# Performance work log

Measured on AMD Instinct MI355X. Metric: run time of the kernel, lower is better.

The kernel has to match this reference:

```python
import jax, jax.numpy as jnp
import numpy as np
import math

L = 3        # n_layers
H = 8        # n_heads
D = 128      # embed_dim
KD = D // H  # key_dim = val_dim = 16
FF = 512     # feed_forward_hidden
B, N = 200, 100
BN = B * N
E = 320000
EPS = 1e-5   # BatchNorm1d eps


def setup_inputs() -> dict:
    key = jax.random.key(0)
    ks = jax.random.split(key, 12)

    def u(k, shape, last):  # torch uniform(-1/sqrt(last), 1/sqrt(last)) init
        s = 1.0 / math.sqrt(last)
        return jax.random.uniform(k, shape, jnp.float32, -s, s)

    x = jax.random.normal(ks[0], (B, N, D), jnp.float32)
    edge_index = jax.random.randint(ks[1], (2, E), 0, BN, jnp.int32)
    return {
        "x": x,
        "edge_index": edge_index,
        "Wq": u(ks[2], (L, H, D, KD), KD),
        "Wk": u(ks[3], (L, H, D, KD), KD),
        "Wv": u(ks[4], (L, H, D, KD), KD),
        "Wout": u(ks[5], (L, H, KD, D), D),
        "bn1_w": jnp.ones((L, D), jnp.float32),
        "bn1_b": jnp.zeros((L, D), jnp.float32),
        "W1": u(ks[6], (L, D, FF), D),
        "b1": u(ks[7], (L, FF), D),
        "W2": u(ks[8], (L, FF, D), FF),
        "b2": u(ks[9], (L, D), FF),
        "bn2_w": jnp.ones((L, D), jnp.float32),
        "bn2_b": jnp.zeros((L, D), jnp.float32),
    }


def _batch_norm(h, w, b):
    # BatchNorm1d over flattened (B*N, D), training-mode batch stats (biased var)
    flat = h.reshape(-1, h.shape[-1])
    mu = flat.mean(axis=0)
    var = flat.var(axis=0)
    y = (flat - mu) / jnp.sqrt(var + EPS) * w + b
    return y.reshape(h.shape)


def _gat_conv(h, src, dst, Wq, Wk, Wv, Wout):
    Bb, Nn, Dd = h.shape
    bn = Bb * Nn
    flat = h.reshape(bn, Dd)
    Hh, _, Kk = Wq.shape
    # faithful to torch: matmul gives [H, BN, K], then raw .view(BN, H, K)
    Q = jnp.einsum('nd,hdk->hnk', flat, Wq).reshape(bn, Hh, Kk)
    Kt = jnp.einsum('nd,hdk->hnk', flat, Wk).reshape(bn, Hh, Kk)
    V = jnp.einsum('nd,hdk->hnk', flat, Wv).reshape(bn, Hh, Kk)
    norm = 1.0 / math.sqrt(Kk)
    # message: Q_j (source) . K_i (target) per edge, per head -> [E, H]
    attn = norm * jnp.sum(Q[src] * Kt[dst], axis=-1)
    # segment softmax over edges grouped by target node (max detached, as in PyG)
    m = jax.lax.stop_gradient(jax.ops.segment_max(attn, dst, num_segments=bn))
    ex = jnp.exp(attn - m[dst])
    s = jax.ops.segment_sum(ex, dst, num_segments=bn)
    a = ex / (s[dst] + 1e-16)
    # weighted V_i scatter-added into target nodes -> [BN, H, K]
    aggr = jax.ops.segment_sum(V[dst] * a[:, :, None], dst, num_segments=bn)
    out = aggr.reshape(bn, Hh * Kk) @ Wout.reshape(Hh * Kk, -1)
    return out.reshape(Bb, Nn, -1)


def reference(x, edge_index, Wq, Wk, Wv, Wout, bn1_w, bn1_b, W1, b1, W2, b2, bn2_w, bn2_b):
    src, dst = edge_index[0], edge_index[1]
    h = x
    for l in range(L):
        h = h + _gat_conv(h, src, dst, Wq[l], Wk[l], Wv[l], Wout[l])
        h = _batch_norm(h, bn1_w[l], bn1_b[l])
        ff = jnp.maximum(h @ W1[l] + b1[l], 0.0) @ W2[l] + b2[l]
        h = h + ff
        h = _batch_norm(h, bn2_w[l], bn2_b[l])
    return h
```

## Files before the change

### kernel.cpp

```cpp
#include <hip/hip_runtime.h>
#include <hip/hip_bf16.h>

#define BN_ 20000
#define D_ 128
#define FF_ 512
#define E_ 320000
#define NBLK 313
#define LSTR 136
#define TSTR 72
#define B2STR 72

typedef __attribute__((ext_vector_type(8))) short bf16x8;
typedef __attribute__((ext_vector_type(4))) float f32x4;

__device__ __forceinline__ unsigned short f2b(float f) {
    unsigned int u = __float_as_uint(f);
    u = (u + 0x7FFFu + ((u >> 16) & 1u)) >> 16;
    return (unsigned short)u;
}

__device__ __forceinline__ void make_ss(const float* __restrict__ acc,
                                        const float* __restrict__ w,
                                        const float* __restrict__ b,
                                        float* __restrict__ ss_sh, int tid) {
    if (tid < 128) {
        if (acc) {
            float s = acc[tid], q = acc[128 + tid];
            float mu  = s * (1.f / 20000.f);
            float var = fmaxf(q * (1.f / 20000.f) - mu * mu, 0.f);
            float rstd  = rsqrtf(var + 1e-5f);
            float scale = w[tid] * rstd;
            ss_sh[tid]       = scale;
            ss_sh[128 + tid] = b[tid] - mu * scale;
        } else {
            ss_sh[tid]       = 1.f;
            ss_sh[128 + tid] = 0.f;
        }
    }
}

__global__ __launch_bounds__(256) void k_prep(const float* __restrict__ Wv,
                                              const float* __restrict__ Wout,
                                              const float* __restrict__ W1,
                                              const float* __restrict__ W2,
                                              const int* __restrict__ dst,
                                              unsigned short* __restrict__ WcT,
                                              unsigned short* __restrict__ WoT,
                                              unsigned short* __restrict__ W1T,
                                              unsigned short* __restrict__ W2T,
                                              float* __restrict__ flag,
                                              float* __restrict__ acc6) {
    const int gid = blockIdx.x * 256 + threadIdx.x;
    const int gs = 1250 * 256;
    for (int idx = gid; idx < 49152; idx += gs) {
        int l = idx / 16384, r = idx % 16384;
        int n = r >> 7, k = r & 127;
        int h = n >> 4, kk = n & 15;
        WcT[idx] = f2b(Wv[((l * 8 + h) * 128 + k) * 16 + kk]);
    }
    for (int idx = gid; idx < 49152; idx += gs) {
        int l = idx / 16384, r = idx % 16384;
        int n = r >> 7, k = r & 127;
        WoT[idx] = f2b(Wout[l * 16384 + k * 128 + n]);
    }
    for (int idx = gid; idx < 196608; idx += gs) {
        int l = idx / 65536, r = idx % 65536;
        int n = r >> 7, k = r & 127;
        W1T[idx] = f2b(W1[l * 65536 + k * 512 + n]);
    }
    for (int idx = gid; idx < 196608; idx += gs) {
        int l = idx / 65536, r = idx % 65536;
        int n = r / 512, k = r % 512;
        W2T[idx] = f2b(W2[l * 65536 + k * 128 + n]);
    }
    if (gid < 1536) acc6[gid] = 0.f;
    if (gid < E_) flag[dst[gid]] = 1.0f;
}


__global__ __launch_bounds__(256) void k_vs(const float* __restrict__ H,
                                            const float* __restrict__ accP,
                                            const float* __restrict__ bnw,
                                            const float* __restrict__ bnb,
                                            const unsigned short* __restrict__ Bt,
                                            unsigned short* __restrict__ Vs) {
    __shared__ unsigned short As[64 * LSTR];
    __shared__ unsigned short Bs[64 * LSTR];
    __shared__ float ss_sh[256];
    const int tid = threadIdx.x;
    const int row0 = blockIdx.x * 64, col0 = blockIdx.y * 64;
    make_ss(accP, bnw, bnb, ss_sh, tid);
    __syncthreads();
#pragma unroll
    for (int it = 0; it < 4; ++it) {
        int idx = tid + it * 256;
        int m = idx >> 4, k0 = (idx & 15) << 3;
        int gr = row0 + m;
        float v[8];
        if (gr < BN_) {
            f32x4 v0 = *(const f32x4*)(H + gr * D_ + k0);
            f32x4 v1 = *(const f32x4*)(H + gr * D_ + k0 + 4);
            v[0] = v0.x; v[1] = v0.y; v[2] = v0.z; v[3] = v0.w;
            v[4] = v1.x; v[5] = v1.y; v[6] = v1.z; v[7] = v1.w;
        } else {
#pragma unroll
            for (int j = 0; j < 8; ++j) v[j] = 0.f;
        }
        unsigned int p[4];
#pragma unroll
        for (int j = 0; j < 4; ++j) {
            unsigned short lo = f2b(v[2 * j] * ss_sh[k0 + 2 * j] + ss_sh[128 + k0 + 2 * j]);
            unsigned short hi = f2b(v[2 * j + 1] * ss_sh[k0 + 2 * j + 1] + ss_sh[128 + k0 + 2 * j + 1]);
            p[j] = (unsigned int)lo | ((unsigned int)hi << 16);
        }
        *(uint4*)&As[m * LSTR + k0] = make_uint4(p[0], p[1], p[2], p[3]);
    }
#pragma unroll
    for (int it = 0; it < 4; ++it) {
        int idx = tid + it * 256;
        int n = idx >> 4, k0 = (idx & 15) << 3;
        *(uint4*)&Bs[n * LSTR + k0] = *(const uint4*)(Bt + (col0 + n) * D_ + k0);
    }
    __syncthreads();
    const int lane = tid & 63, wave = tid >> 6;
    const int l16 = lane & 15, quad = lane >> 4;
    const int wm = (wave >> 1) * 32, wn = (wave & 1) * 32;
    f32x4 acc[2][2] = {};
#pragma unroll
    for (int kb = 0; kb < 128; kb += 32) {
        bf16x8 a0 = *(bf16x8*)&As[(wm + l16) * LSTR + kb + quad * 8];
        bf16x8 a1 = *(bf16x8*)&As[(wm + 16 + l16) * LSTR + kb + quad * 8];
        bf16x8 b0 = *(bf16x8*)&Bs[(wn + l16) * LSTR + kb + quad * 8];
        bf16x8 b1 = *(bf16x8*)&Bs[(wn + 16 + l16) * LSTR + kb + quad * 8];
        acc[0][0] = __builtin_amdgcn_mfma_f32_16x16x32_bf16(a0, b0, acc[0][0], 0, 0, 0);
        acc[0][1] = __builtin_amdgcn_mfma_f32_16x16x32_bf16(a0, b1, acc[0][1], 0, 0, 0);
        acc[1][0] = __builtin_amdgcn_mfma_f32_16x16x32_bf16(a1, b0, acc[1][0], 0, 0, 0);
        acc[1][1] = __builtin_amdgcn_mfma_f32_16x16x32_bf16(a1, b1, acc[1][1], 0, 0, 0);
    }
#pragma unroll
    for (int i = 0; i < 2; ++i)
#pragma unroll
        for (int j = 0; j < 2; ++j) {
            int gc = col0 + wn + j * 16 + l16;
            int h = gc >> 4, kk = gc & 15;
#pragma unroll
            for (int r = 0; r < 4; ++r) {
                int gr = row0 + wm + i * 16 + quad * 4 + r;
                if (gr < BN_) Vs[h * (BN_ * 16) + gr * 16 + kk] = f2b(acc[i][j][r]);
            }
        }
}

__global__ __launch_bounds__(256) void k_out(const unsigned short* __restrict__ Vs,
                                             const unsigned short* __restrict__ Bt,
                                             const float* __restrict__ H,
                                             const float* __restrict__ accP,
                                             const float* __restrict__ bnw,
                                             const float* __restrict__ bnb,
                                             const float* __restrict__ flag,
                                             float* __restrict__ H1,
                                             float* __restrict__ accO) {
    __shared__ unsigned short As[64 * LSTR];
    __shared__ unsigned short Bs[64 * LSTR];
    __shared__ float ss_sh[256];
    const int tid = threadIdx.x;
    const int row0 = blockIdx.x * 64, col0 = blockIdx.y * 64;
    make_ss(accP, bnw, bnb, ss_sh, tid);
#pragma unroll
    for (int it = 0; it < 4; ++it) {
        int idx = tid + it * 256;
        int m = idx >> 4, k0 = (idx & 15) << 3;
        int gr = row0 + m;
        uint4 w = make_uint4(0u, 0u, 0u, 0u);
        if (gr < BN_) w = *(const uint4*)(Vs + gr * D_ + k0);
        *(uint4*)&As[m * LSTR + k0] = w;
    }
#pragma unroll
    for (int it = 0; it < 4; ++it) {
        int idx = tid + it * 256;
        int n = idx >> 4, k0 = (idx & 15) << 3;
        *(uint4*)&Bs[n * LSTR + k0] = *(const uint4*)(Bt + (col0 + n) * D_ + k0);
    }
    __syncthreads();
    const int lane = tid & 63, wave = tid >> 6;
    const int l16 = lane & 15, quad = lane >> 4;
    const int wm = (wave >> 1) * 32, wn = (wave & 1) * 32;
    f32x4 acc[2][2] = {};
#pragma unroll
    for (int kb = 0; kb < 128; kb += 32) {
        bf16x8 a0 = *(bf16x8*)&As[(wm + l16) * LSTR + kb + quad * 8];
        bf16x8 a1 = *(bf16x8*)&As[(wm + 16 + l16) * LSTR + kb + quad * 8];
        bf16x8 b0 = *(bf16x8*)&Bs[(wn + l16) * LSTR + kb + quad * 8];
        bf16x8 b1 = *(bf16x8*)&Bs[(wn + 16 + l16) * LSTR + kb + quad * 8];
        acc[0][0] = __builtin_amdgcn_mfma_f32_16x16x32_bf16(a0, b0, acc[0][0], 0, 0, 0);
        acc[0][1] = __builtin_amdgcn_mfma_f32_16x16x32_bf16(a0, b1, acc[0][1], 0, 0, 0);
        acc[1][0] = __builtin_amdgcn_mfma_f32_16x16x32_bf16(a1, b0, acc[1][0], 0, 0, 0);
        acc[1][1] = __builtin_amdgcn_mfma_f32_16x16x32_bf16(a1, b1, acc[1][1], 0, 0, 0);
    }
    __syncthreads();
    float* Sred = (float*)As;
    float* Qred = (float*)Bs;
    const int slot = (wave >> 1) * 4 + quad;
#pragma unroll
    for (int j = 0; j < 2; ++j) {
        int gc = col0 + wn + j * 16 + l16;
        float sc = ss_sh[gc & 127];
        float sh = ss_sh[128 + (gc & 127)];
        float cs = 0.f, cq = 0.f;
#pragma unroll
        for (int i = 0; i < 2; ++i)
#pragma unroll
            for (int r = 0; r < 4; ++r) {
                int gr = row0 + wm + i * 16 + quad * 4 + r;
                if (gr < BN_) {
                    float z = H[gr * D_ + gc] * sc + sh;
                    float o = z + flag[gr] * acc[i][j][r];
                    H1[gr * D_ + gc] = o;
                    cs += o; cq += o * o;
                }
            }
        Sred[(wn + j * 16 + l16) * 8 + slot] = cs;
        Qred[(wn + j * 16 + l16) * 8 + slot] = cq;
    }
    __syncthreads();
    if (tid < 64) {
        float s = 0.f, q = 0.f;
#pragma unroll
        for (int t = 0; t < 8; ++t) { s += Sred[tid * 8 + t]; q += Qred[tid * 8 + t]; }
        atomicAdd(&accO[col0 + tid], s);
        atomicAdd(&accO[128 + col0 + tid], q);
    }
}

__global__ __launch_bounds__(256) void k_ff(const float* __restrict__ H1,
                                            const float* __restrict__ accP,
                                            const float* __restrict__ bnw,
                                            const float* __restrict__ bnb,
                                            const unsigned short* __restrict__ W1t,
                                            const float* __restrict__ b1l,
                                            const unsigned short* __restrict__ W2t,
                                            const float* __restrict__ b2l,
                                            float* __restrict__ H2,
                                            float* __restrict__ accO) {
    __shared__ unsigned short As[64 * LSTR];
    __shared__ unsigned short Bs[64 * LSTR];
    __shared__ unsigned short B2[128 * B2STR];
    __shared__ unsigned short Tch[64 * TSTR];
    __shared__ float ss_sh[256];
    const int tid = threadIdx.x;
    const int row0 = blockIdx.x * 64;
    make_ss(accP, bnw, bnb, ss_sh, tid);
    __syncthreads();
#pragma unroll
    for (int it = 0; it < 4; ++it) {
        int idx = tid + it * 256;
        int m = idx >> 4, k0 = (idx & 15) << 3;
        int gr = row0 + m;
        float v[8];
        if (gr < BN_) {
            f32x4 v0 = *(const f32x4*)(H1 + gr * D_ + k0);
            f32x4 v1 = *(const f32x4*)(H1 + gr * D_ + k0 + 4);
            v[0] = v0.x; v[1] = v0.y; v[2] = v0.z; v[3] = v0.w;
            v[4] = v1.x; v[5] = v1.y; v[6] = v1.z; v[7] = v1.w;
        } else {
#pragma unroll
            for (int j = 0; j < 8; ++j) v[j] = 0.f;
        }
        unsigned int p[4];
#pragma unroll
        for (int j = 0; j < 4; ++j) {
            unsigned short lo = f2b(v[2 * j] * ss_sh[k0 + 2 * j] + ss_sh[128 + k0 + 2 * j]);
            unsigned short hi = f2b(v[2 * j + 1] * ss_sh[k0 + 2 * j + 1] + ss_sh[128 + k0 + 2 * j + 1]);
            p[j] = (unsigned int)lo | ((unsigned int)hi << 16);
        }
        *(uint4*)&As[m * LSTR + k0] = make_uint4(p[0], p[1], p[2], p[3]);
    }
    const int lane = tid & 63, wave = tid >> 6;
    const int l16 = lane & 15, quad = lane >> 4;
    const int wm = (wave >> 1) * 32;
    const int wn = (wave & 1) * 32;
    const int wn2 = (wave & 1) * 64;
    f32x4 acc2[2][4] = {};
    for (int c = 0; c < 8; ++c) {
        const int cb = c * 64;
        __syncthreads();
#pragma unroll
        for (int it = 0; it < 4; ++it) {
            int idx = tid + it * 256;
            int n = idx >> 4, k0 = (idx & 15) << 3;
            *(uint4*)&Bs[n * LSTR + k0] = *(const uint4*)(W1t + (cb + n) * D_ + k0);
        }
#pragma unroll
        for (int it = 0; it < 4; ++it) {
            int idx = tid + it * 256;
            int n = idx >> 3, k0 = (idx & 7) << 3;
            *(uint4*)&B2[n * B2STR + k0] = *(const uint4*)(W2t + n * FF_ + cb + k0);
        }
        __syncthreads();
        f32x4 acc1[2][2] = {};
#pragma unroll
        for (int kb = 0; kb < 128; kb += 32) {
            bf16x8 a0 = *(bf16x8*)&As[(wm + l16) * LSTR + kb + quad * 8];
            bf16x8 a1 = *(bf16x8*)&As[(wm + 16 + l16) * LSTR + kb + quad * 8];
            bf16x8 b0 = *(bf16x8*)&Bs[(wn + l16) * LSTR + kb + quad * 8];
            bf16x8 b1 = *(bf16x8*)&Bs[(wn + 16 + l16) * LSTR + kb + quad * 8];
            acc1[0][0] = __builtin_amdgcn_mfma_f32_16x16x32_bf16(a0, b0, acc1[0][0], 0, 0, 0);
            acc1[0][1] = __builtin_amdgcn_mfma_f32_16x16x32_bf16(a0, b1, acc1[0][1], 0, 0, 0);
            acc1[1][0] = __builtin_amdgcn_mfma_f32_16x16x32_bf16(a1, b0, acc1[1][0], 0, 0, 0);
            acc1[1][1] = __builtin_amdgcn_mfma_f32_16x16x32_bf16(a1, b1, acc1[1][1], 0, 0, 0);
        }
#pragma unroll
        for (int j = 0; j < 2; ++j) {
            int lc = wn + j * 16 + l16;
            float bb = b1l[cb + lc];
#pragma unroll
            for (int i = 0; i < 2; ++i)
#pragma unroll
                for (int r = 0; r < 4; ++r)
                    Tch[(wm + i * 16 + quad * 4 + r) * TSTR + lc] =
                        f2b(fmaxf(acc1[i][j][r] + bb, 0.f));
        }
        __syncthreads();
#pragma unroll
        for (int kb = 0; kb < 64; kb += 32) {
            bf16x8 a0 = *(bf16x8*)&Tch[(wm + l16) * TSTR + kb + quad * 8];
            bf16x8 a1 = *(bf16x8*)&Tch[(wm + 16 + l16) * TSTR + kb + quad * 8];
#pragma unroll
            for (int j2 = 0; j2 < 4; ++j2) {
                bf16x8 b = *(bf16x8*)&B2[(wn2 + j2 * 16 + l16) * B2STR + kb + quad * 8];
                acc2[0][j2] = __builtin_amdgcn_mfma_f32_16x16x32_bf16(a0, b, acc2[0][j2], 0, 0, 0);
                acc2[1][j2] = __builtin_amdgcn_mfma_f32_16x16x32_bf16(a1, b, acc2[1][j2], 0, 0, 0);
            }
        }
    }
    __syncthreads();
    float* Sred = (float*)As;
    float* Qred = (float*)Bs;
    const int slot = (wave >> 1) * 4 + quad;
#pragma unroll
    for (int j2 = 0; j2 < 4; ++j2) {
        int gc = wn2 + j2 * 16 + l16;
        float sc = ss_sh[gc], sh = ss_sh[128 + gc], bb = b2l[gc];
        float cs = 0.f, cq = 0.f;
#pragma unroll
        for (int i = 0; i < 2; ++i)
#pragma unroll
            for (int r = 0; r < 4; ++r) {
                int gr = row0 + wm + i * 16 + quad * 4 + r;
                if (gr < BN_) {
                    float o = H1[gr * D_ + gc] * sc + sh + acc2[i][j2][r] + bb;
                    H2[gr * D_ + gc] = o;
                    cs += o; cq += o * o;
                }
            }
        Sred[gc * 8 + slot] = cs;
        Qred[gc * 8 + slot] = cq;
    }
    __syncthreads();
    if (tid < 128) {
        float s = 0.f, q = 0.f;
#pragma unroll
        for (int t = 0; t < 8; ++t) { s += Sred[tid * 8 + t]; q += Qred[tid * 8 + t]; }
        atomicAdd(&accO[tid], s);
        atomicAdd(&accO[128 + tid], q);
    }
}

__global__ __launch_bounds__(256) void k_apply(const float4* __restrict__ H2,
                                               const float* __restrict__ accP,
                                               const float* __restrict__ bnw,
                                               const float* __restrict__ bnb,
                                               float4* __restrict__ out) {
    __shared__ float ss_sh[256];
    make_ss(accP, bnw, bnb, ss_sh, threadIdx.x);
    __syncthreads();
    int i = blockIdx.x * 256 + threadIdx.x;
    if (i >= BN_ * D_ / 4) return;
    int c = (i & 31) << 2;
    float4 v = H2[i];
    v.x = v.x * ss_sh[c + 0] + ss_sh[128 + c + 0];
    v.y = v.y * ss_sh[c + 1] + ss_sh[128 + c + 1];
    v.z = v.z * ss_sh[c + 2] + ss_sh[128 + c + 2];
    v.w = v.w * ss_sh[c + 3] + ss_sh[128 + c + 3];
    out[i] = v;
}


extern "C" void kernel_launch(void* const* d_in, const int* in_sizes, int n_in,
                              void* d_out, int out_size, void* d_ws, size_t ws_size,
                              hipStream_t stream) {
    (void)in_sizes; (void)n_in; (void)out_size; (void)ws_size;
    const float* x    = (const float*)d_in[0];
    const int*   edge = (const int*)d_in[1];
    const float* Wv   = (const float*)d_in[4];
    const float* Wout = (const float*)d_in[5];
    const float* bn1w = (const float*)d_in[6];
    const float* bn1b = (const float*)d_in[7];
    const float* W1   = (const float*)d_in[8];
    const float* b1   = (const float*)d_in[9];
    const float* W2   = (const float*)d_in[10];
    const float* b2   = (const float*)d_in[11];
    const float* bn2w = (const float*)d_in[12];
    const float* bn2b = (const float*)d_in[13];

    float* ws   = (float*)d_ws;
    float* bufA = ws;
    float* bufB = ws + 2560000;
    float* flag = ws + 5120000;
    float* acc6 = ws + 5140000;
    unsigned short* Vs  = (unsigned short*)(ws + 5141536);
    unsigned short* WcT = (unsigned short*)(ws + 6421536);
    unsigned short* WoT = (unsigned short*)(ws + 6446112);
    unsigned short* W1T = (unsigned short*)(ws + 6470688);
    unsigned short* W2T = (unsigned short*)(ws + 6568992);

    k_prep<<<1250, 256, 0, stream>>>(Wv, Wout, W1, W2, edge + E_,
                                     WcT, WoT, W1T, W2T, flag, acc6);

    for (int l = 0; l < 3; ++l) {
        const float* Hc   = (l == 0) ? x : bufA;
        const float* accP = (l == 0) ? nullptr : acc6 + (2 * l - 1) * 256;
        float* acc1p = acc6 + (2 * l) * 256;
        float* acc2p = acc6 + (2 * l + 1) * 256;
        const float* bw  = bn2w + (l ? (l - 1) * 128 : 0);
        const float* bbv = bn2b + (l ? (l - 1) * 128 : 0);
        k_vs<<<dim3(NBLK, 2), 256, 0, stream>>>(Hc, accP, bw, bbv,
                                                WcT + l * 16384, Vs);
        k_out<<<dim3(NBLK, 2), 256, 0, stream>>>(Vs, WoT + l * 16384, Hc, accP,
                                                 bw, bbv, flag, bufB, acc1p);
        k_ff<<<NBLK, 256, 0, stream>>>(bufB, acc1p, bn1w + l * 128, bn1b + l * 128,
                                       W1T + l * 65536, b1 + l * 512,
                                       W2T + l * 65536, b2 + l * 128, bufA, acc2p);
    }
    k_apply<<<2500, 256, 0, stream>>>((const float4*)bufA, acc6 + 5 * 256,
                                      bn2w + 256, bn2b + 256, (float4*)d_out);
}
```

Baseline: 253.1 us.

## Compute full 128-column output per block in k_vs and k_out

```diff
diff --git a/kernel.cpp b/kernel.cpp
--- a/kernel.cpp
+++ b/kernel.cpp
@@ -88,7 +88,7 @@
     __shared__ unsigned short Bs[64 * LSTR];
     __shared__ float ss_sh[256];
     const int tid = threadIdx.x;
-    const int row0 = blockIdx.x * 64, col0 = blockIdx.y * 64;
+    const int row0 = blockIdx.x * 64;
     make_ss(accP, bnw, bnb, ss_sh, tid);
     __syncthreads();
 #pragma unroll
@@ -115,40 +115,45 @@
         }
         *(uint4*)&As[m * LSTR + k0] = make_uint4(p[0], p[1], p[2], p[3]);
     }
-#pragma unroll
-    for (int it = 0; it < 4; ++it) {
-        int idx = tid + it * 256;
-        int n = idx >> 4, k0 = (idx & 15) << 3;
-        *(uint4*)&Bs[n * LSTR + k0] = *(const uint4*)(Bt + (col0 + n) * D_ + k0);
-    }
-    __syncthreads();
     const int lane = tid & 63, wave = tid >> 6;
     const int l16 = lane & 15, quad = lane >> 4;
     const int wm = (wave >> 1) * 32, wn = (wave & 1) * 32;
-    f32x4 acc[2][2] = {};
-#pragma unroll
-    for (int kb = 0; kb < 128; kb += 32) {
-        bf16x8 a0 = *(bf16x8*)&As[(wm + l16) * LSTR + kb + quad * 8];
-        bf16x8 a1 = *(bf16x8*)&As[(wm + 16 + l16) * LSTR + kb + quad * 8];
-        bf16x8 b0 = *(bf16x8*)&Bs[(wn + l16) * LSTR + kb + quad * 8];
-        bf16x8 b1 = *(bf16x8*)&Bs[(wn + 16 + l16) * LSTR + kb + quad * 8];
-        acc[0][0] = __builtin_amdgcn_mfma_f32_16x16x32_bf16(a0, b0, acc[0][0], 0, 0, 0);
-        acc[0][1] = __builtin_amdgcn_mfma_f32_16x16x32_bf16(a0, b1, acc[0][1], 0, 0, 0);
-        acc[1][0] = __builtin_amdgcn_mfma_f32_16x16x32_bf16(a1, b0, acc[1][0], 0, 0, 0);
-        acc[1][1] = __builtin_amdgcn_mfma_f32_16x16x32_bf16(a1, b1, acc[1][1], 0, 0, 0);
-    }
-#pragma unroll
-    for (int i = 0; i < 2; ++i)
-#pragma unroll
-        for (int j = 0; j < 2; ++j) {
-            int gc = col0 + wn + j * 16 + l16;
-            int h = gc >> 4, kk = gc & 15;
-#pragma unroll
-            for (int r = 0; r < 4; ++r) {
-                int gr = row0 + wm + i * 16 + quad * 4 + r;
-                if (gr < BN_) Vs[h * (BN_ * 16) + gr * 16 + kk] = f2b(acc[i][j][r]);
+#pragma unroll
+    for (int half = 0; half < 2; ++half) {
+        const int col0 = half * 64;
+        if (half) __syncthreads();
+#pragma unroll
+        for (int it = 0; it < 4; ++it) {
+            int idx = tid + it * 256;
+            int n = idx >> 4, k0 = (idx & 15) << 3;
+            *(uint4*)&Bs[n * LSTR + k0] = *(const uint4*)(Bt + (col0 + n) * D_ + k0);
+        }
+        __syncthreads();
+        f32x4 acc[2][2] = {};
+#pragma unroll
+        for (int kb = 0; kb < 128; kb += 32) {
+            bf16x8 a0 = *(bf16x8*)&As[(wm + l16) * LSTR + kb + quad * 8];
+            bf16x8 a1 = *(bf16x8*)&As[(wm + 16 + l16) * LSTR + kb + quad * 8];
+            bf16x8 b0 = *(bf16x8*)&Bs[(wn + l16) * LSTR + kb + quad * 8];
+            bf16x8 b1 = *(bf16x8*)&Bs[(wn + 16 + l16) * LSTR + kb + quad * 8];
+            acc[0][0] = __builtin_amdgcn_mfma_f32_16x16x32_bf16(a0, b0, acc[0][0], 0, 0, 0);
+            acc[0][1] = __builtin_amdgcn_mfma_f32_16x16x32_bf16(a0, b1, acc[0][1], 0, 0, 0);
+            acc[1][0] = __builtin_amdgcn_mfma_f32_16x16x32_bf16(a1, b0, acc[1][0], 0, 0, 0);
+            acc[1][1] = __builtin_amdgcn_mfma_f32_16x16x32_bf16(a1, b1, acc[1][1], 0, 0, 0);
+        }
+#pragma unroll
+        for (int i = 0; i < 2; ++i)
+#pragma unroll
+            for (int j = 0; j < 2; ++j) {
+                int gc = col0 + wn + j * 16 + l16;
+                int h = gc >> 4, kk = gc & 15;
+#pragma unroll
+                for (int r = 0; r < 4; ++r) {
+                    int gr = row0 + wm + i * 16 + quad * 4 + r;
+                    if (gr < BN_) Vs[h * (BN_ * 16) + gr * 16 + kk] = f2b(acc[i][j][r]);
+                }
             }
-        }
+    }
 }
 
 __global__ __launch_bounds__(256) void k_out(const unsigned short* __restrict__ Vs,
@@ -164,7 +169,7 @@
     __shared__ unsigned short Bs[64 * LSTR];
     __shared__ float ss_sh[256];
     const int tid = threadIdx.x;
-    const int row0 = blockIdx.x * 64, col0 = blockIdx.y * 64;
+    const int row0 = blockIdx.x * 64;
     make_ss(accP, bnw, bnb, ss_sh, tid);
 #pragma unroll
     for (int it = 0; it < 4; ++it) {
@@ -175,60 +180,66 @@
         if (gr < BN_) w = *(const uint4*)(Vs + gr * D_ + k0);
         *(uint4*)&As[m * LSTR + k0] = w;
     }
-#pragma unroll
-    for (int it = 0; it < 4; ++it) {
-        int idx = tid + it * 256;
-        int n = idx >> 4, k0 = (idx & 15) << 3;
-        *(uint4*)&Bs[n * LSTR + k0] = *(const uint4*)(Bt + (col0 + n) * D_ + k0);
-    }
-    __syncthreads();
     const int lane = tid & 63, wave = tid >> 6;
     const int l16 = lane & 15, quad = lane >> 4;
     const int wm = (wave >> 1) * 32, wn = (wave & 1) * 32;
-    f32x4 acc[2][2] = {};
-#pragma unroll
-    for (int kb = 0; kb < 128; kb += 32) {
-        bf16x8 a0 = *(bf16x8*)&As[(wm + l16) * LSTR + kb + quad * 8];
-        bf16x8 a1 = *(bf16x8*)&As[(wm + 16 + l16) * LSTR + kb + quad * 8];
-        bf16x8 b0 = *(bf16x8*)&Bs[(wn + l16) * LSTR + kb + quad * 8];
-        bf16x8 b1 = *(bf16x8*)&Bs[(wn + 16 + l16) * LSTR + kb + quad * 8];
-        acc[0][0] = __builtin_amdgcn_mfma_f32_16x16x32_bf16(a0, b0, acc[0][0], 0, 0, 0);
-        acc[0][1] = __builtin_amdgcn_mfma_f32_16x16x32_bf16(a0, b1, acc[0][1], 0, 0, 0);
-        acc[1][0] = __builtin_amdgcn_mfma_f32_16x16x32_bf16(a1, b0, acc[1][0], 0, 0, 0);
-        acc[1][1] = __builtin_amdgcn_mfma_f32_16x16x32_bf16(a1, b1, acc[1][1], 0, 0, 0);
+    f32x4 acc3[2][2][2] = {};
+#pragma unroll
+    for (int half = 0; half < 2; ++half) {
+        const int col0 = half * 64;
+        if (half) __syncthreads();
+#pragma unroll
+        for (int it = 0; it < 4; ++it) {
+            int idx = tid + it * 256;
+            int n = idx >> 4, k0 = (idx & 15) << 3;
+            *(uint4*)&Bs[n * LSTR + k0] = *(const uint4*)(Bt + (col0 + n) * D_ + k0);
+        }
+        __syncthreads();
+#pragma unroll
+        for (int kb = 0; kb < 128; kb += 32) {
+            bf16x8 a0 = *(bf16x8*)&As[(wm + l16) * LSTR + kb + quad * 8];
+            bf16x8 a1 = *(bf16x8*)&As[(wm + 16 + l16) * LSTR + kb + quad * 8];
+            bf16x8 b0 = *(bf16x8*)&Bs[(wn + l16) * LSTR + kb + quad * 8];
+            bf16x8 b1 = *(bf16x8*)&Bs[(wn + 16 + l16) * LSTR + kb + quad * 8];
+            acc3[half][0][0] = __builtin_amdgcn_mfma_f32_16x16x32_bf16(a0, b0, acc3[half][0][0], 0, 0, 0);
+            acc3[half][0][1] = __builtin_amdgcn_mfma_f32_16x16x32_bf16(a0, b1, acc3[half][0][1], 0, 0, 0);
+            acc3[half][1][0] = __builtin_amdgcn_mfma_f32_16x16x32_bf16(a1, b0, acc3[half][1][0], 0, 0, 0);
+            acc3[half][1][1] = __builtin_amdgcn_mfma_f32_16x16x32_bf16(a1, b1, acc3[half][1][1], 0, 0, 0);
+        }
     }
     __syncthreads();
     float* Sred = (float*)As;
     float* Qred = (float*)Bs;
     const int slot = (wave >> 1) * 4 + quad;
 #pragma unroll
-    for (int j = 0; j < 2; ++j) {
-        int gc = col0 + wn + j * 16 + l16;
-        float sc = ss_sh[gc & 127];
-        float sh = ss_sh[128 + (gc & 127)];
-        float cs = 0.f, cq = 0.f;
-#pragma unroll
-        for (int i = 0; i < 2; ++i)
-#pragma unroll
-            for (int r = 0; r < 4; ++r) {
-                int gr = row0 + wm + i * 16 + quad * 4 + r;
-                if (gr < BN_) {
-                    float z = H[gr * D_ + gc] * sc + sh;
-                    float o = z + flag[gr] * acc[i][j][r];
-                    H1[gr * D_ + gc] = o;
-                    cs += o; cq += o * o;
+    for (int half = 0; half < 2; ++half)
+#pragma unroll
+        for (int j = 0; j < 2; ++j) {
+            int gc = half * 64 + wn + j * 16 + l16;
+            float sc = ss_sh[gc], sh = ss_sh[128 + gc];
+            float cs = 0.f, cq = 0.f;
+#pragma unroll
+            for (int i = 0; i < 2; ++i)
+#pragma unroll
+                for (int r = 0; r < 4; ++r) {
+                    int gr = row0 + wm + i * 16 + quad * 4 + r;
+                    if (gr < BN_) {
+                        float z = H[gr * D_ + gc] * sc + sh;
+                        float o = z + flag[gr] * acc3[half][i][j][r];
+                        H1[gr * D_ + gc] = o;
+                        cs += o; cq += o * o;
+                    }
                 }
-            }
-        Sred[(wn + j * 16 + l16) * 8 + slot] = cs;
-        Qred[(wn + j * 16 + l16) * 8 + slot] = cq;
-    }
-    __syncthreads();
-    if (tid < 64) {
+            Sred[gc * 8 + slot] = cs;
+            Qred[gc * 8 + slot] = cq;
+        }
+    __syncthreads();
+    if (tid < 128) {
         float s = 0.f, q = 0.f;
 #pragma unroll
         for (int t = 0; t < 8; ++t) { s += Sred[tid * 8 + t]; q += Qred[tid * 8 + t]; }
-        atomicAdd(&accO[col0 + tid], s);
-        atomicAdd(&accO[128 + col0 + tid], q);
+        atomicAdd(&accO[tid], s);
+        atomicAdd(&accO[128 + tid], q);
     }
 }
 
@@ -424,10 +435,9 @@
         float* acc2p = acc6 + (2 * l + 1) * 256;
         const float* bw  = bn2w + (l ? (l - 1) * 128 : 0);
         const float* bbv = bn2b + (l ? (l - 1) * 128 : 0);
-        k_vs<<<dim3(NBLK, 2), 256, 0, stream>>>(Hc, accP, bw, bbv,
-                                                WcT + l * 16384, Vs);
-        k_out<<<dim3(NBLK, 2), 256, 0, stream>>>(Vs, WoT + l * 16384, Hc, accP,
-                                                 bw, bbv, flag, bufB, acc1p);
+        k_vs<<<NBLK, 256, 0, stream>>>(Hc, accP, bw, bbv, WcT + l * 16384, Vs);
+        k_out<<<NBLK, 256, 0, stream>>>(Vs, WoT + l * 16384, Hc, accP,
+                                        bw, bbv, flag, bufB, acc1p);
         k_ff<<<NBLK, 256, 0, stream>>>(bufB, acc1p, bn1w + l * 128, bn1b + l * 128,
                                        W1T + l * 65536, b1 + l * 512,
                                        W2T + l * 65536, b2 + l * 128, bufA, acc2p);
```

Measured after the change: 253.8 us. No clear change (+0.3%).
